# Kernel optimization log

Measured on AMD Instinct MI355X. Metric: run time of the kernel, lower is better.

## Reference

```python
import jax, jax.numpy as jnp
import numpy as np

N = 4
SEGMENTS = 16
IN_F = 256
OUT_F = 256
BATCH = 512


def chebyshev_lobatto(n):
    # Chebyshev-Lobatto interpolation nodes on [-1, 1]
    k = jnp.arange(n, dtype=jnp.float32)
    return -jnp.cos(jnp.pi * k / (n - 1))


def lagrange_basis(x, nodes):
    # x: [B, In]; returns basis values [B, In, n]
    n = nodes.shape[0]
    cols = []
    for j in range(n):  # n is a small static constant (4)
        terms = [(x - nodes[m]) / (nodes[j] - nodes[m]) for m in range(n) if m != j]
        cols.append(jnp.prod(jnp.stack(terms, axis=0), axis=0))
    return jnp.stack(cols, axis=-1)


def setup_inputs() -> dict:
    key = jax.random.key(0)
    k1, k2 = jax.random.split(key)
    x = jax.random.uniform(k1, (BATCH, IN_F), dtype=jnp.float32, minval=-1.0, maxval=1.0)
    w = jax.random.uniform(
        k2, (OUT_F, IN_F, (N - 1) * SEGMENTS + 1), dtype=jnp.float32, minval=-1.0, maxval=1.0
    )
    return {"x": x, "w": w, "n": N, "segments": SEGMENTS}


def reference(x, w, n, segments):
    nodes = chebyshev_lobatto(n)
    # segment id per element, clamped to [0, segments-1]
    id_min = jnp.clip(((x + 1.0) / 2.0 * segments).astype(jnp.int32), 0, segments - 1)
    id_max = id_min + 1
    wid_min = id_min * (n - 1)  # start of weight slice; slice length == n
    # segment boundaries in x-space: eta(i) = i/segments * 2 - 1
    x_min = id_min.astype(x.dtype) / segments * 2.0 - 1.0
    x_max = id_max.astype(x.dtype) / segments * 2.0 - 1.0
    # rescale x into [-1, 1] within its segment
    x_in = 2.0 * (x - x_min) / (x_max - x_min) - 1.0
    basis = lagrange_basis(x_in, nodes)  # [B, In, n]
    # gather per-element weight slice: w_g[b,i,j,o] = w[o, i, wid_min[b,i]+j]
    idx = wid_min[..., None] + jnp.arange(n)  # [B, In, n]
    w_t = jnp.transpose(w, (1, 2, 0))  # [In, K, Out]
    in_f = w.shape[1]
    w_g = w_t[jnp.arange(in_f)[None, :, None], idx]  # [B, In, n, Out]
    # interpolate and sum over in_features (matches einsum 'ijk,jkli->jl')
    return jnp.einsum("bin,bino->bo", basis, w_g)
```

## Files before the change

kernel.cpp:

```cpp
#include <hip/hip_runtime.h>


typedef _Float16 h2 __attribute__((ext_vector_type(2)));

#define INF     256
#define OUTF    256
#define WSTRIDE 49
#define OSTRIDE (INF * WSTRIDE)
#define NSPLIT  16
#define IPB     16
#define WE_UINTS (256 * 128 * 64)

#define GLOAD16(gptr, lptr)                                                         \
  __builtin_amdgcn_global_load_lds(                                                 \
      (const __attribute__((address_space(1))) unsigned int*)(gptr),                \
      (__attribute__((address_space(3))) unsigned int*)(lptr), 16, 0, 0)

__global__ __launch_bounds__(256)
void pp_expand(const float* __restrict__ w, unsigned int* __restrict__ we) {
    __shared__ float lds_w[2][3136];

    const int tid   = threadIdx.x;
    const int op    = blockIdx.x >> 1;
    const int ihalf = blockIdx.x & 1;
    const int o0    = op * 2;

    for (int c = 0; c < 2; ++c) {
        const int i_c = ihalf * 128 + c * 64;

        #pragma unroll
        for (int oe = 0; oe < 2; ++oe) {
            const float* src = w + (size_t)(o0 + oe) * OSTRIDE + (size_t)i_c * WSTRIDE;
            #pragma unroll
            for (int it = 0; it < 4; ++it) {
                int u = it * 256 + tid;
                if (u < 784)
                    GLOAD16(src + u * 4, &lds_w[oe][u * 4]);
            }
        }
        __syncthreads();

        #pragma unroll
        for (int r = 0; r < 4; ++r) {
            int item = r * 256 + tid;
            int il = item >> 4, s = item & 15;
            const float* t0 = &lds_w[0][il * 49 + 3 * s];
            const float* t1 = &lds_w[1][il * 49 + 3 * s];
            uint4 v;
            v.x = __builtin_bit_cast(unsigned int,
                      __builtin_amdgcn_cvt_pkrtz(t0[0], t0[1]));
            v.y = __builtin_bit_cast(unsigned int,
                      __builtin_amdgcn_cvt_pkrtz(t0[2], t0[3]));
            v.z = __builtin_bit_cast(unsigned int,
                      __builtin_amdgcn_cvt_pkrtz(t1[0], t1[1]));
            v.w = __builtin_bit_cast(unsigned int,
                      __builtin_amdgcn_cvt_pkrtz(t1[2], t1[3]));
            *(uint4*)(we + (((size_t)(i_c + il) * 128 + op) * 16 + s) * 4) = v;
        }
        __syncthreads();
    }
}

__global__ __launch_bounds__(256, 2)
void pp_partial(const float* __restrict__ x, const unsigned int* __restrict__ we,
                float* __restrict__ part) {
    __shared__ unsigned int smem[16384];

    const int tid  = threadIdx.x;
    const int wave = tid >> 6, lane = tid & 63;
    const int isplit  = blockIdx.x;
    const int i_base  = isplit * IPB;
    const int op_base = blockIdx.y * 16;
    const int o_base  = blockIdx.y * 32;
    const int b_base  = blockIdx.z * 64;
    const int b = b_base + lane;

    #pragma unroll
    for (int it = 0; it < 16; ++it) {
        int u = it * 256 + tid;
        int iloc = u >> 8, opl = (u >> 4) & 15, s = u & 15;
        const unsigned int* gp =
            we + (((size_t)(i_base + iloc) * 128 + op_base + opl) * 16 + s) * 4;
        GLOAD16(gp, &smem[u * 4]);
    }

    int sseg[IPB]; h2 cA[IPB], cB[IPB];
    {
        const float4* xp = (const float4*)(x + (size_t)b * INF + i_base);
        float4 x0 = xp[0], x1 = xp[1], x2 = xp[2], x3 = xp[3];
        float xs[16] = {x0.x, x0.y, x0.z, x0.w, x1.x, x1.y, x1.z, x1.w,
                        x2.x, x2.y, x2.z, x2.w, x3.x, x3.y, x3.z, x3.w};
        #pragma unroll
        for (int i = 0; i < IPB; ++i) {
            float xx = xs[i];
            int id = (int)((xx + 1.0f) * 8.0f);
            id = id < 0 ? 0 : (id > 15 ? 15 : id);
            float u = (xx - ((float)id * 0.125f - 1.0f)) * 16.0f - 1.0f;
            float a = u + 1.0f, b2 = u + 0.5f, cc = u - 0.5f, d = u - 1.0f;
            float c0 = b2 * cc * d  * (-2.0f / 3.0f);
            float c1 = a  * cc * d  * ( 4.0f / 3.0f);
            float c2 = a  * b2 * d  * (-4.0f / 3.0f);
            float c3 = a  * b2 * cc * ( 2.0f / 3.0f);
            h2 pA; pA[0] = (_Float16)c0; pA[1] = (_Float16)c1;
            h2 pB; pB[0] = (_Float16)c2; pB[1] = (_Float16)c3;
            cA[i] = pA; cB[i] = pB; sseg[i] = id;
        }
    }

    __syncthreads();

    float acc[8];
    #pragma unroll
    for (int q = 0; q < 8; ++q) acc[q] = 0.0f;

    #pragma unroll
    for (int i = 0; i < IPB; ++i) {
        const unsigned int* p = &smem[(i * 16 + wave * 4) * 64 + sseg[i] * 4];
        #pragma unroll
        for (int pq = 0; pq < 4; ++pq) {
            uint4 v = *(const uint4*)(p + pq * 64);
            acc[2*pq]   = __builtin_amdgcn_fdot2(__builtin_bit_cast(h2, v.x), cA[i],
                                                 acc[2*pq],   false);
            acc[2*pq]   = __builtin_amdgcn_fdot2(__builtin_bit_cast(h2, v.y), cB[i],
                                                 acc[2*pq],   false);
            acc[2*pq+1] = __builtin_amdgcn_fdot2(__builtin_bit_cast(h2, v.z), cA[i],
                                                 acc[2*pq+1], false);
            acc[2*pq+1] = __builtin_amdgcn_fdot2(__builtin_bit_cast(h2, v.w), cB[i],
                                                 acc[2*pq+1], false);
        }
    }

    __syncthreads();
    float* smf = (float*)smem;
    #pragma unroll
    for (int q = 0; q < 8; ++q)
        smf[lane * 33 + wave * 8 + q] = acc[q];
    __syncthreads();

    const int qo = tid & 7;
    const int g  = tid >> 3;
    #pragma unroll
    for (int r = 0; r < 2; ++r) {
        int b_l = g + 32 * r;
        float4 v;
        v.x = smf[b_l * 33 + qo * 4 + 0];
        v.y = smf[b_l * 33 + qo * 4 + 1];
        v.z = smf[b_l * 33 + qo * 4 + 2];
        v.w = smf[b_l * 33 + qo * 4 + 3];
        *(float4*)(part + (size_t)isplit * (512 * 256)
                        + (size_t)(b_base + b_l) * 256 + o_base + qo * 4) = v;
    }
}

__global__ __launch_bounds__(256)
void pp_reduce(const float* __restrict__ part, float* __restrict__ out) {
    const size_t off4 = (size_t)blockIdx.x * 256 + threadIdx.x;
    const float4* p4 = (const float4*)part;
    float4 s = make_float4(0.f, 0.f, 0.f, 0.f);
    #pragma unroll
    for (int k = 0; k < NSPLIT; ++k) {
        float4 v = p4[(size_t)k * (512 * 64) + off4];
        s.x += v.x; s.y += v.y; s.z += v.z; s.w += v.w;
    }
    ((float4*)out)[off4] = s;
}

extern "C" void kernel_launch(void* const* d_in, const int* in_sizes, int n_in,
                              void* d_out, int out_size, void* d_ws, size_t ws_size,
                              hipStream_t stream) {
    const float* x = (const float*)d_in[0];
    const float* w = (const float*)d_in[1];
    float* out = (float*)d_out;
    unsigned int* we = (unsigned int*)d_ws;
    float* part = (float*)((char*)d_ws + (size_t)WE_UINTS * 4);
    (void)ws_size; (void)n_in; (void)in_sizes; (void)out_size;

    pp_expand<<<dim3(256), 256, 0, stream>>>(w, we);
    pp_partial<<<dim3(NSPLIT, 8, 8), 256, 0, stream>>>(x, we, part);
    pp_reduce<<<dim3(128), 256, 0, stream>>>(part, out);
}
```

Baseline: 85.30 us.

## Replace split-K partial buffer and reduce kernel with atomic accumulation

```diff
diff --git a/kernel.cpp b/kernel.cpp
--- a/kernel.cpp
+++ b/kernel.cpp
@@ -17,10 +17,17 @@
       (__attribute__((address_space(3))) unsigned int*)(lptr), 16, 0, 0)
 
 __global__ __launch_bounds__(256)
-void pp_expand(const float* __restrict__ w, unsigned int* __restrict__ we) {
+void pp_expand(const float* __restrict__ w, unsigned int* __restrict__ we,
+               float* __restrict__ out) {
     __shared__ float lds_w[2][3136];
 
     const int tid   = threadIdx.x;
+
+    {
+        size_t idx = ((size_t)blockIdx.x * 256 + tid) * 2;
+        *(float2*)(out + idx) = make_float2(0.f, 0.f);
+    }
+
     const int op    = blockIdx.x >> 1;
     const int ihalf = blockIdx.x & 1;
     const int o0    = op * 2;
@@ -61,23 +68,25 @@
     }
 }
 
-__global__ __launch_bounds__(256, 2)
+__global__ __launch_bounds__(512, 4)
 void pp_partial(const float* __restrict__ x, const unsigned int* __restrict__ we,
-                float* __restrict__ part) {
+                float* __restrict__ out) {
     __shared__ unsigned int smem[16384];
 
     const int tid  = threadIdx.x;
     const int wave = tid >> 6, lane = tid & 63;
+    const int osub = wave & 3;
+    const int bsub = wave >> 2;
     const int isplit  = blockIdx.x;
     const int i_base  = isplit * IPB;
     const int op_base = blockIdx.y * 16;
     const int o_base  = blockIdx.y * 32;
-    const int b_base  = blockIdx.z * 64;
-    const int b = b_base + lane;
+    const int b_base  = blockIdx.z * 128;
+    const int b = b_base + bsub * 64 + lane;
 
     #pragma unroll
-    for (int it = 0; it < 16; ++it) {
-        int u = it * 256 + tid;
+    for (int it = 0; it < 8; ++it) {
+        int u = it * 512 + tid;
         int iloc = u >> 8, opl = (u >> 4) & 15, s = u & 15;
         const unsigned int* gp =
             we + (((size_t)(i_base + iloc) * 128 + op_base + opl) * 16 + s) * 4;
@@ -115,7 +124,7 @@
 
     #pragma unroll
     for (int i = 0; i < IPB; ++i) {
-        const unsigned int* p = &smem[(i * 16 + wave * 4) * 64 + sseg[i] * 4];
+        const unsigned int* p = &smem[(i * 16 + osub * 4) * 64 + sseg[i] * 4];
         #pragma unroll
         for (int pq = 0; pq < 4; ++pq) {
             uint4 v = *(const uint4*)(p + pq * 64);
@@ -132,37 +141,27 @@
 
     __syncthreads();
     float* smf = (float*)smem;
+    const int b_l0 = bsub * 64 + lane;
     #pragma unroll
     for (int q = 0; q < 8; ++q)
-        smf[lane * 33 + wave * 8 + q] = acc[q];
+        smf[b_l0 * 33 + osub * 8 + q] = acc[q];
     __syncthreads();
 
     const int qo = tid & 7;
     const int g  = tid >> 3;
     #pragma unroll
     for (int r = 0; r < 2; ++r) {
-        int b_l = g + 32 * r;
-        float4 v;
-        v.x = smf[b_l * 33 + qo * 4 + 0];
-        v.y = smf[b_l * 33 + qo * 4 + 1];
-        v.z = smf[b_l * 33 + qo * 4 + 2];
-        v.w = smf[b_l * 33 + qo * 4 + 3];
-        *(float4*)(part + (size_t)isplit * (512 * 256)
-                        + (size_t)(b_base + b_l) * 256 + o_base + qo * 4) = v;
+        int b_l = g + 64 * r;
+        float vx = smf[b_l * 33 + qo * 4 + 0];
+        float vy = smf[b_l * 33 + qo * 4 + 1];
+        float vz = smf[b_l * 33 + qo * 4 + 2];
+        float vw = smf[b_l * 33 + qo * 4 + 3];
+        float* dst = out + (size_t)(b_base + b_l) * 256 + o_base + qo * 4;
+        atomicAdd(dst + 0, vx);
+        atomicAdd(dst + 1, vy);
+        atomicAdd(dst + 2, vz);
+        atomicAdd(dst + 3, vw);
     }
-}
-
-__global__ __launch_bounds__(256)
-void pp_reduce(const float* __restrict__ part, float* __restrict__ out) {
-    const size_t off4 = (size_t)blockIdx.x * 256 + threadIdx.x;
-    const float4* p4 = (const float4*)part;
-    float4 s = make_float4(0.f, 0.f, 0.f, 0.f);
-    #pragma unroll
-    for (int k = 0; k < NSPLIT; ++k) {
-        float4 v = p4[(size_t)k * (512 * 64) + off4];
-        s.x += v.x; s.y += v.y; s.z += v.z; s.w += v.w;
-    }
-    ((float4*)out)[off4] = s;
 }
 
 extern "C" void kernel_launch(void* const* d_in, const int* in_sizes, int n_in,
@@ -172,10 +171,8 @@
     const float* w = (const float*)d_in[1];
     float* out = (float*)d_out;
     unsigned int* we = (unsigned int*)d_ws;
-    float* part = (float*)((char*)d_ws + (size_t)WE_UINTS * 4);
     (void)ws_size; (void)n_in; (void)in_sizes; (void)out_size;
 
-    pp_expand<<<dim3(256), 256, 0, stream>>>(w, we);
-    pp_partial<<<dim3(NSPLIT, 8, 8), 256, 0, stream>>>(x, we, part);
-    pp_reduce<<<dim3(128), 256, 0, stream>>>(part, out);
+    pp_expand<<<dim3(256), 256, 0, stream>>>(w, we, out);
+    pp_partial<<<dim3(NSPLIT, 8, 4), 512, 0, stream>>>(x, we, out);
 }
```

Measured after the change: 106.1 us. 1.24x slower.
